# Performance work log

Hardware: AMD Instinct MI355X
Metric: run time of the kernel (lower is better)

## Reference

```python
import jax, jax.numpy as jnp
import numpy as np

C = 512
GROUPS = 32
EPS = 1e-6


def group_norm(x, w, b):
    # x: [B, C, H, W]
    B, Cc, H, W = x.shape
    xg = x.reshape(B, GROUPS, Cc // GROUPS, H, W)
    mean = xg.mean(axis=(2, 3, 4), keepdims=True)
    var = xg.var(axis=(2, 3, 4), keepdims=True)
    xn = (xg - mean) * jax.lax.rsqrt(var + EPS)
    xn = xn.reshape(B, Cc, H, W)
    return xn * w[None, :, None, None] + b[None, :, None, None]


def conv1x1(x, w, b):
    # 1x1 conv == per-pixel linear: w [Cout, Cin], x [B, Cin, H, W]
    return jnp.einsum('oc,bchw->bohw', w, x) + b[None, :, None, None]


def setup_inputs() -> dict:
    key = jax.random.key(0)
    ks = jax.random.split(key, 11)
    B, H, W = 4, 64, 64
    s = 1.0 / np.sqrt(C)
    return {
        'x': jax.random.normal(ks[0], (B, C, H, W), dtype=jnp.float32),
        'gn_w': jnp.ones((C,), dtype=jnp.float32),
        'gn_b': jnp.zeros((C,), dtype=jnp.float32),
        'wq': jax.random.normal(ks[1], (C, C), dtype=jnp.float32) * s,
        'bq': jnp.zeros((C,), dtype=jnp.float32),
        'wk': jax.random.normal(ks[2], (C, C), dtype=jnp.float32) * s,
        'bk': jnp.zeros((C,), dtype=jnp.float32),
        'wv': jax.random.normal(ks[3], (C, C), dtype=jnp.float32) * s,
        'bv': jnp.zeros((C,), dtype=jnp.float32),
        'wo': jax.random.normal(ks[4], (C, C), dtype=jnp.float32) * s,
        'bo': jnp.zeros((C,), dtype=jnp.float32),
    }


def reference(x, gn_w, gn_b, wq, bq, wk, bk, wv, bv, wo, bo):
    B, Cc, H, W = x.shape
    scale = Cc ** (-0.5)
    xn = group_norm(x, gn_w, gn_b)
    q = conv1x1(xn, wq, bq).reshape(B, Cc, H * W)
    k = conv1x1(xn, wk, bk).reshape(B, Cc, H * W)
    v = conv1x1(xn, wv, bv).reshape(B, Cc, H * W)
    attn = jax.nn.softmax(jnp.einsum('bci,bcj->bij', q, k) * scale, axis=2)
    out = jnp.einsum('bij,bcj->bci', attn, v).reshape(B, Cc, H, W)
    out = conv1x1(out, wo, bo)
    return x + out
```

## Files before the change

### kernel.cpp

```cpp
#include <hip/hip_runtime.h>

#define NB 4
#define CC 512
#define NSP 4096
#define NGRP 32

using bf16x8 = __attribute__((ext_vector_type(8))) __bf16;
using f32x4  = __attribute__((ext_vector_type(4))) float;

__device__ __forceinline__ unsigned short f2bf(float f) {
  union { float f; unsigned int u; } v; v.f = f;
  unsigned int r = v.u + 0x7fffu + ((v.u >> 16) & 1u);
  return (unsigned short)(r >> 16);
}
__device__ __forceinline__ float bf2f(unsigned short h) {
  union { unsigned int u; float f; } v; v.u = ((unsigned int)h) << 16;
  return v.f;
}

__global__ __launch_bounds__(256) void cvt_w_kernel(const float* __restrict__ wq,
    const float* __restrict__ wk, const float* __restrict__ wv,
    const float* __restrict__ wo, const float* __restrict__ bq,
    const float* __restrict__ bk, unsigned short* __restrict__ wqk,
    unsigned short* __restrict__ wv_bf, unsigned short* __restrict__ wo_bf,
    float* __restrict__ bias_qk, float scale) {
  int i = blockIdx.x * 256 + threadIdx.x;
  wqk[i]          = f2bf(wq[i] * scale);
  wqk[i + 262144] = f2bf(wk[i]);
  wv_bf[i] = f2bf(wv[i]);
  wo_bf[i] = f2bf(wo[i]);
  if (i < 512)        bias_qk[i] = bq[i] * scale;
  else if (i < 1024)  bias_qk[i] = bk[i - 512];
}

__global__ __launch_bounds__(256) void gn_stats_kernel(const float* __restrict__ x,
                                                       float* __restrict__ stats) {
  const int b = blockIdx.x >> 5, g = blockIdx.x & 31;
  const float4* p = reinterpret_cast<const float4*>(x + ((size_t)b * CC + g * 16) * NSP);
  float s = 0.f, ss = 0.f;
  for (int i = threadIdx.x; i < 16384; i += 256) {
    float4 v = p[i];
    s  += v.x + v.y + v.z + v.w;
    ss += v.x * v.x + v.y * v.y + v.z * v.z + v.w * v.w;
  }
  __shared__ float rs[4], rss[4];
  #pragma unroll
  for (int o = 32; o >= 1; o >>= 1) { s += __shfl_down(s, o); ss += __shfl_down(ss, o); }
  if ((threadIdx.x & 63) == 0) { rs[threadIdx.x >> 6] = s; rss[threadIdx.x >> 6] = ss; }
  __syncthreads();
  if (threadIdx.x == 0) {
    s = rs[0] + rs[1] + rs[2] + rs[3];
    ss = rss[0] + rss[1] + rss[2] + rss[3];
    float mean = s * (1.f / 65536.f);
    float var = ss * (1.f / 65536.f) - mean * mean;
    stats[blockIdx.x * 2 + 0] = mean;
    stats[blockIdx.x * 2 + 1] = rsqrtf(var + 1e-6f);
  }
}

__global__ __launch_bounds__(256) void gn_apply_kernel(const float* __restrict__ x,
    const float* __restrict__ stats, const float* __restrict__ gw,
    const float* __restrict__ gb, unsigned short* __restrict__ xnT) {
  const int b = blockIdx.z, c0 = blockIdx.y * 32, n0 = blockIdx.x * 32;
  __shared__ unsigned short tile[32][33];
  const int tx = threadIdx.x & 31, ty = threadIdx.x >> 5;
  #pragma unroll
  for (int r = 0; r < 4; ++r) {
    const int cl = ty + r * 8;
    const int c = c0 + cl;
    const int g = c >> 4;
    const float mean = stats[(b * 32 + g) * 2];
    const float rstd = stats[(b * 32 + g) * 2 + 1];
    const float sc = rstd * gw[c];
    const float sh = gb[c] - mean * sc;
    const float v = x[((size_t)b * CC + c) * NSP + n0 + tx];
    tile[cl][tx] = f2bf(v * sc + sh);
  }
  __syncthreads();
  #pragma unroll
  for (int r = 0; r < 4; ++r) {
    const int nl = ty + r * 8;
    xnT[((size_t)b * NSP + n0 + nl) * CC + c0 + tx] = tile[tx][nl];
  }
}

__global__ __launch_bounds__(256) void sum_reduce_kernel(const float* __restrict__ part,
                                                         float* __restrict__ invl) {
  const int row = blockIdx.x * 4 + (threadIdx.x >> 6);
  const int lane = threadIdx.x & 63;
  float v = part[((size_t)row << 6) + lane];
  #pragma unroll
  for (int msk = 1; msk <= 32; msk <<= 1) v += __shfl_xor(v, msk);
  if (lane == 0) invl[row] = 1.f / v;
}

template<int BIAS, int OMODE, bool RESID>
__global__ __launch_bounds__(256) void gemm2(
    const unsigned short* __restrict__ A, const unsigned short* __restrict__ B,
    const float* __restrict__ bias, const float* __restrict__ resid,
    void* __restrict__ Cout, void* __restrict__ Cout2,
    int M, int N, int K, float scale,
    long long sAb, long long sBb, long long sCb, long long sRb) {
  __shared__ __align__(16) unsigned short sA[2][128 * 64];
  __shared__ __align__(16) unsigned short sB[2][128 * 64];
  const int tid = threadIdx.x;
  const int lane = tid & 63;
  const int wid  = tid >> 6;

  const unsigned nwg = gridDim.x * gridDim.y * gridDim.z;
  unsigned lin = blockIdx.x + gridDim.x * (blockIdx.y + gridDim.y * blockIdx.z);
  lin = (lin & 7) * (nwg >> 3) + (lin >> 3);
  const int bn = lin % gridDim.x;
  const unsigned t2 = lin / gridDim.x;
  const int bm = t2 % gridDim.y;
  const int b  = t2 / gridDim.y;

  const unsigned short* Ab = A + (size_t)b * sAb + (size_t)bm * 128 * K;
  const unsigned short* Bb = B + (size_t)b * sBb + (size_t)bn * 128 * K;
  const int wm = wid >> 1, wn = wid & 1;
  const int l15 = lane & 15, h = lane >> 4;

  f32x4 acc[4][4] = {};

  auto stage = [&](int buf, int k0) {
    #pragma unroll
    for (int it = 0; it < 4; ++it) {
      const int o  = (it * 256 + tid) * 16;
      const int r  = o >> 7;
      const int c2 = (o & 127) ^ ((r & 7) << 4);
      __builtin_amdgcn_global_load_lds(
          (const __attribute__((address_space(1))) void*)((const char*)(Ab + (size_t)r * K + k0) + c2),
          (__attribute__((address_space(3))) void*)((char*)sA[buf] + o), 16, 0, 0);
      __builtin_amdgcn_global_load_lds(
          (const __attribute__((address_space(1))) void*)((const char*)(Bb + (size_t)r * K + k0) + c2),
          (__attribute__((address_space(3))) void*)((char*)sB[buf] + o), 16, 0, 0);
    }
  };

  int abase[4], bbase[4];
  #pragma unroll
  for (int i = 0; i < 4; ++i) {
    const int ar = wm * 64 + i * 16 + l15;
    abase[i] = ar * 128 + (((ar & 7) << 4) ^ (h << 4));
    const int br = wn * 64 + i * 16 + l15;
    bbase[i] = br * 128 + (((br & 7) << 4) ^ (h << 4));
  }

  stage(0, 0);
  const int NT = K >> 6;
  #pragma unroll 1
  for (int t = 0; t < NT; ++t) {
    const int cur = t & 1;
    if (t + 1 < NT) {
      stage(cur ^ 1, (t + 1) << 6);
      asm volatile("s_waitcnt vmcnt(8)" ::: "memory");
    } else {
      asm volatile("s_waitcnt vmcnt(0)" ::: "memory");
    }
    __builtin_amdgcn_sched_barrier(0);
    __builtin_amdgcn_s_barrier();
    __builtin_amdgcn_sched_barrier(0);

    const char* cA = (const char*)sA[cur];
    const char* cB = (const char*)sB[cur];
    #pragma unroll
    for (int kk = 0; kk < 2; ++kk) {
      bf16x8 af[4], bfr[4];
      #pragma unroll
      for (int m = 0; m < 4; ++m)
        af[m] = *reinterpret_cast<const bf16x8*>(cA + (abase[m] ^ (kk << 6)));
      #pragma unroll
      for (int n = 0; n < 4; ++n)
        bfr[n] = *reinterpret_cast<const bf16x8*>(cB + (bbase[n] ^ (kk << 6)));
      #pragma unroll
      for (int m = 0; m < 4; ++m)
        #pragma unroll
        for (int n = 0; n < 4; ++n)
          acc[m][n] = __builtin_amdgcn_mfma_f32_16x16x32_bf16(af[m], bfr[n], acc[m][n], 0, 0, 0);
    }
    __builtin_amdgcn_sched_barrier(0);
    __builtin_amdgcn_s_barrier();
    __builtin_amdgcn_sched_barrier(0);
  }

  const size_t cb = (size_t)b * sCb;
  #pragma unroll
  for (int m = 0; m < 4; ++m) {
    #pragma unroll
    for (int r = 0; r < 4; ++r) {
      const int row = bm * 128 + wm * 64 + m * 16 + h * 4 + r;
      #pragma unroll
      for (int n = 0; n < 4; ++n) {
        const int col = bn * 128 + wn * 64 + n * 16 + l15;
        float vv = acc[m][n][r];
        if constexpr (BIAS == 1) vv += bias[row];
        if constexpr (BIAS == 2) vv += bias[col];
        vv *= scale;
        if constexpr (RESID) vv += resid[(size_t)b * sRb + (size_t)row * N + col];
        if constexpr (OMODE == 0) {
          ((float*)Cout)[cb + (size_t)row * N + col] = vv;
        } else if constexpr (OMODE == 1) {
          ((unsigned short*)Cout)[cb + (size_t)row * N + col] = f2bf(vv);
        } else {
          unsigned short* dst = (col < 512) ? (unsigned short*)Cout : (unsigned short*)Cout2;
          dst[cb + (size_t)row * 512 + (col & 511)] = f2bf(vv);
        }
      }
    }
  }
}

template<int BN, int WMs, int OMODE>
__global__ __launch_bounds__(512) void gemm8p(
    const unsigned short* __restrict__ A, const unsigned short* __restrict__ B,
    void* __restrict__ Cout, const float* __restrict__ invl_in,
    float* __restrict__ part_out, int N, int K, int lda, int ldb,
    long long sAb, long long sBb, long long sCb) {
  constexpr int WNs = 8 / WMs;
  constexpr int WR = 256 / WMs;
  constexpr int M_REP = WR / 16;
  constexpr int BH = BN / 128;
  __shared__ __align__(16) unsigned short sA[2][256 * 64];
  __shared__ __align__(16) unsigned short sB[2][BN * 64];
  const int tid = threadIdx.x;
  const int lane = tid & 63;
  const int wid  = tid >> 6;

  const unsigned nwg = gridDim.x * gridDim.y * gridDim.z;
  unsigned lin = blockIdx.x + gridDim.x * (blockIdx.y + gridDim.y * blockIdx.z);
  lin = (lin & 7) * (nwg >> 3) + (lin >> 3);
  const int bn = lin % gridDim.x;
  const unsigned t2 = lin / gridDim.x;
  const int bm = t2 % gridDim.y;
  const int b  = t2 / gridDim.y;

  const unsigned short* Ab = A + (size_t)b * sAb + (size_t)bm * 256 * lda;
  const unsigned short* Bb = B + (size_t)b * sBb + (size_t)bn * BN * ldb;
  const int wm = wid / WNs, wn = wid % WNs;
  const int l15 = lane & 15, h = lane >> 4;

  auto stage_half = [&](const unsigned short* gbase, int ld, int k0, unsigned short* lbase) {
    #pragma unroll
    for (int it = 0; it < 2; ++it) {
      const int o = (it * 512 + tid) * 16;
      const int r = o >> 7;
      const int c2 = (o & 127) ^ ((r & 7) << 4);
      __builtin_amdgcn_global_load_lds(
          (const __attribute__((address_space(1))) void*)((const char*)(gbase + (size_t)r * ld + k0) + c2),
          (__attribute__((address_space(3))) void*)((char*)lbase + o), 16, 0, 0);
    }
  };

  int abase[M_REP], bbase[4];
  #pragma unroll
  for (int i = 0; i < M_REP; ++i) {
    const int ar = wm * WR + i * 16 + l15;
    abase[i] = ar * 128 + (((ar & 7) << 4) ^ (h << 4));
  }
  #pragma unroll
  for (int i = 0; i < 4; ++i) {
    const int br = wn * 64 + i * 16 + l15;
    bbase[i] = br * 128 + (((br & 7) << 4) ^ (h << 4));
  }

  f32x4 acc[M_REP][4] = {};
  const int NT = K >> 6;

  stage_half(Ab, lda, 0, &sA[0][0]);
  stage_half(Ab + (size_t)128 * lda, lda, 0, &sA[0][128 * 64]);
  #pragma unroll
  for (int hs = 0; hs < BH; ++hs)
    stage_half(Bb + (size_t)hs * 128 * ldb, ldb, 0, &sB[0][hs * 128 * 64]);
  #pragma unroll
  for (int hs = 0; hs < BH; ++hs)
    stage_half(Bb + (size_t)hs * 128 * ldb, ldb, 64, &sB[1][hs * 128 * 64]);
  if constexpr (BH == 2) asm volatile("s_waitcnt vmcnt(4)" ::: "memory");
  else                   asm volatile("s_waitcnt vmcnt(2)" ::: "memory");
  __builtin_amdgcn_s_barrier();

  #pragma unroll 1
  for (int u = 0; u < NT; u += 2) {
    const bool lastit = (u + 2 >= NT);
    #pragma unroll
    for (int half = 0; half < 2; ++half) {
      const char* cA = (const char*)sA[half];
      const char* cB = (const char*)sB[half];
      bf16x8 bfr[2][4];
      #pragma unroll
      for (int p = 0; p < M_REP / 2; ++p) {
        if (p == 0) {
          #pragma unroll
          for (int kk = 0; kk < 2; ++kk)
            #pragma unroll
            for (int n = 0; n < 4; ++n)
              bfr[kk][n] = *reinterpret_cast<const bf16x8*>(cB + (bbase[n] ^ (kk << 6)));
        }
        bf16x8 af[2][2];
        #pragma unroll
        for (int i = 0; i < 2; ++i)
          #pragma unroll
          for (int kk = 0; kk < 2; ++kk)
            af[kk][i] = *reinterpret_cast<const bf16x8*>(cA + (abase[2 * p + i] ^ (kk << 6)));

        const int ph = half * (M_REP / 2) + p;
        if constexpr (M_REP == 8) {
          if (ph == 0)      stage_half(Ab, lda, (u + 1) << 6, &sA[1][0]);
          else if (ph == 1) stage_half(Ab + (size_t)128 * lda, lda, (u + 1) << 6, &sA[1][128 * 64]);
          else if (ph == 2) { if (u + 2 < NT) stage_half(Bb, ldb, (u + 2) << 6, &sB[0][0]); }
          else if (ph == 3) { if (u + 2 < NT) stage_half(Bb + (size_t)128 * ldb, ldb, (u + 2) << 6, &sB[0][128 * 64]); }
          else if (ph == 4) { if (u + 2 < NT) stage_half(Ab, lda, (u + 2) << 6, &sA[0][0]); }
          else if (ph == 5) { if (u + 2 < NT) stage_half(Ab + (size_t)128 * lda, lda, (u + 2) << 6, &sA[0][128 * 64]); }
          else if (ph == 6) { if (u + 3 < NT) stage_half(Bb, ldb, (u + 3) << 6, &sB[1][0]); }
          else              { if (u + 3 < NT) stage_half(Bb + (size_t)128 * ldb, ldb, (u + 3) << 6, &sB[1][128 * 64]); }
        } else {
          if (ph == 0) {
            stage_half(Ab, lda, (u + 1) << 6, &sA[1][0]);
            stage_half(Ab + (size_t)128 * lda, lda, (u + 1) << 6, &sA[1][128 * 64]);
          } else if (ph == 1) {
            if (u + 2 < NT) stage_half(Bb, ldb, (u + 2) << 6, &sB[0][0]);
          } else if (ph == 2) {
            if (u + 2 < NT) {
              stage_half(Ab, lda, (u + 2) << 6, &sA[0][0]);
              stage_half(Ab + (size_t)128 * lda, lda, (u + 2) << 6, &sA[0][128 * 64]);
            }
          } else {
            if (u + 3 < NT) stage_half(Bb, ldb, (u + 3) << 6, &sB[1][0]);
          }
        }

        __builtin_amdgcn_s_barrier();
        asm volatile("s_waitcnt lgkmcnt(0)");
        __builtin_amdgcn_s_setprio(1);
        #pragma unroll
        for (int i = 0; i < 2; ++i)
          #pragma unroll
          for (int n = 0; n < 4; ++n)
            #pragma unroll
            for (int kk = 0; kk < 2; ++kk)
              acc[2 * p + i][n] = __builtin_amdgcn_mfma_f32_16x16x32_bf16(
                  af[kk][i], bfr[kk][n], acc[2 * p + i][n], 0, 0, 0);
        __builtin_amdgcn_s_setprio(0);
        if (p == M_REP / 2 - 1) {
          if (half == 0) {
            if (lastit) asm volatile("s_waitcnt vmcnt(0)" ::: "memory");
            else if constexpr (BH == 2) asm volatile("s_waitcnt vmcnt(4)" ::: "memory");
            else                        asm volatile("s_waitcnt vmcnt(2)" ::: "memory");
          } else if (!lastit) {
            if constexpr (BH == 2) asm volatile("s_waitcnt vmcnt(4)" ::: "memory");
            else                   asm volatile("s_waitcnt vmcnt(2)" ::: "memory");
          }
        }
        __builtin_amdgcn_s_barrier();
      }
    }
  }

  const size_t cb = (size_t)b * sCb;
  if constexpr (OMODE == 2) {
    unsigned short* outh = (unsigned short*)Cout;
    #pragma unroll
    for (int m = 0; m < M_REP; ++m) {
      #pragma unroll
      for (int r = 0; r < 4; ++r) {
        const int row = bm * 256 + wm * WR + m * 16 + h * 4 + r;
        float se = 0.f;
        #pragma unroll
        for (int n = 0; n < 4; ++n) {
          const int col = bn * BN + wn * 64 + n * 16 + l15;
          unsigned short pb = f2bf(__expf(fminf(acc[m][n][r], 80.f)));
          outh[cb + (size_t)row * N + col] = pb;
          se += bf2f(pb);
        }
        #pragma unroll
        for (int msk = 1; msk <= 8; msk <<= 1) se += __shfl_xor(se, msk);
        if (l15 == 0)
          part_out[(((size_t)b * NSP + row) << 6) + bn * (BN / 64) + wn] = se;
      }
    }
  } else {
    unsigned short* outh = (unsigned short*)Cout;
    #pragma unroll
    for (int m = 0; m < M_REP; ++m) {
      #pragma unroll
      for (int r = 0; r < 4; ++r) {
        const int row = bm * 256 + wm * WR + m * 16 + h * 4 + r;
        const float il = invl_in[(size_t)b * NSP + row];
        #pragma unroll
        for (int n = 0; n < 4; ++n) {
          const int col = bn * BN + wn * 64 + n * 16 + l15;
          outh[cb + (size_t)row * N + col] = f2bf(acc[m][n][r] * il);
        }
      }
    }
  }
}

extern "C" void kernel_launch(void* const* d_in, const int* in_sizes, int n_in,
                              void* d_out, int out_size, void* d_ws, size_t ws_size,
                              hipStream_t stream) {
  const float* x    = (const float*)d_in[0];
  const float* gn_w = (const float*)d_in[1];
  const float* gn_b = (const float*)d_in[2];
  const float* wq   = (const float*)d_in[3];
  const float* bq   = (const float*)d_in[4];
  const float* wk   = (const float*)d_in[5];
  const float* bk   = (const float*)d_in[6];
  const float* wv   = (const float*)d_in[7];
  const float* bv   = (const float*)d_in[8];
  const float* wo   = (const float*)d_in[9];
  const float* bo   = (const float*)d_in[10];
  float* out = (float*)d_out;

  char* ws = (char*)d_ws;
  const size_t NC = (size_t)NSP * CC;
  unsigned short* wqk_bf = (unsigned short*)ws;
  unsigned short* wv_bf  = wqk_bf + 524288;
  unsigned short* wo_bf  = wv_bf + 262144;
  float* bias_qk = (float*)(wo_bf + 262144);
  float* gstats  = bias_qk + 1024;
  unsigned short* xnT = (unsigned short*)(gstats + 512);
  unsigned short* qT  = xnT + NB * NC;
  unsigned short* kT  = qT + NB * NC;
  unsigned short* vC  = kT + NB * NC;
  unsigned short* aoutT = vC + NB * NC;
  unsigned short* S = aoutT + NB * NC;
  float* part = (float*)(S + (size_t)NB * NSP * NSP);
  float* invl = part + ((size_t)NB * NSP << 6);

  const float scale = 0.04419417382415922f;
  const long long SS = (long long)NSP * NSP;

  cvt_w_kernel<<<1024, 256, 0, stream>>>(wq, wk, wv, wo, bq, bk,
                                         wqk_bf, wv_bf, wo_bf, bias_qk, scale);
  gn_stats_kernel<<<NB * NGRP, 256, 0, stream>>>(x, gstats);
  gn_apply_kernel<<<dim3(NSP / 32, CC / 32, NB), 256, 0, stream>>>(x, gstats, gn_w, gn_b, xnT);

  gemm2<2, 3, false><<<dim3(1024 / 128, NSP / 128, NB), 256, 0, stream>>>(
      xnT, wqk_bf, bias_qk, nullptr, qT, kT, NSP, 1024, CC, 1.0f, NC, 0, NC, 0);
  gemm2<1, 1, false><<<dim3(NSP / 128, CC / 128, NB), 256, 0, stream>>>(
      wv_bf, xnT, bv, nullptr, vC, nullptr, CC, NSP, CC, 1.0f, 0, NC, NC, 0);

  gemm8p<256, 2, 2><<<dim3(NSP / 256, NSP / 256, NB), 512, 0, stream>>>(
      qT, kT, S, nullptr, part, NSP, CC, CC, CC, NC, NC, SS);
  sum_reduce_kernel<<<NB * NSP / 4, 256, 0, stream>>>(part, invl);
  gemm8p<128, 4, 1><<<dim3(CC / 128, NSP / 256, NB), 512, 0, stream>>>(
      S, vC, aoutT, invl, nullptr, CC, NSP, NSP, NSP, SS, NC, NC);

  gemm2<1, 0, true><<<dim3(NSP / 128, CC / 128, NB), 256, 0, stream>>>(
      wo_bf, aoutT, bo, x, out, nullptr, CC, NSP, CC, 1.0f, 0, NC, NC, NC);
}
```

Baseline: 280.5 us.

## Transpose attention GEMMs to emit vectorized ushort4 stores and halve partial sums

Swaps the operand roles of the QK^T and PV GEMMs so the score matrix is computed transposed (rows index keys, columns index queries). Each thread can then write four consecutive bf16 exponentials as one ushort4 store instead of scattered 2-byte stores. Row-sum partials now accumulate along the key dimension in registers with fewer shuffles, giving 32 partials per row instead of 64, and the reduction kernel is adjusted to match. The PV GEMM grid and operand strides are reworked to consume the transposed S layout. The risk is that the new index mapping does not line up exactly with the S layout and part-slot count the kernels assume.

```diff
diff --git a/kernel.cpp b/kernel.cpp
--- a/kernel.cpp
+++ b/kernel.cpp
@@ -86,12 +86,12 @@
 
 __global__ __launch_bounds__(256) void sum_reduce_kernel(const float* __restrict__ part,
                                                          float* __restrict__ invl) {
-  const int row = blockIdx.x * 4 + (threadIdx.x >> 6);
-  const int lane = threadIdx.x & 63;
-  float v = part[((size_t)row << 6) + lane];
-  #pragma unroll
-  for (int msk = 1; msk <= 32; msk <<= 1) v += __shfl_xor(v, msk);
-  if (lane == 0) invl[row] = 1.f / v;
+  const int row = blockIdx.x * 8 + (threadIdx.x >> 5);
+  const int sl = threadIdx.x & 31;
+  float v = part[((size_t)row << 5) + sl];
+  #pragma unroll
+  for (int msk = 1; msk <= 16; msk <<= 1) v += __shfl_xor(v, msk);
+  if (sl == 0) invl[row] = 1.f / v;
 }
 
 template<int BIAS, int OMODE, bool RESID>
@@ -358,38 +358,49 @@
   const size_t cb = (size_t)b * sCb;
   if constexpr (OMODE == 2) {
     unsigned short* outh = (unsigned short*)Cout;
+    float pn[4] = {0.f, 0.f, 0.f, 0.f};
     #pragma unroll
     for (int m = 0; m < M_REP; ++m) {
-      #pragma unroll
-      for (int r = 0; r < 4; ++r) {
-        const int row = bm * 256 + wm * WR + m * 16 + h * 4 + r;
-        float se = 0.f;
-        #pragma unroll
-        for (int n = 0; n < 4; ++n) {
-          const int col = bn * BN + wn * 64 + n * 16 + l15;
-          unsigned short pb = f2bf(__expf(fminf(acc[m][n][r], 80.f)));
-          outh[cb + (size_t)row * N + col] = pb;
-          se += bf2f(pb);
-        }
-        #pragma unroll
-        for (int msk = 1; msk <= 8; msk <<= 1) se += __shfl_xor(se, msk);
-        if (l15 == 0)
-          part_out[(((size_t)b * NSP + row) << 6) + bn * (BN / 64) + wn] = se;
+      const int j0 = bm * 256 + wm * WR + m * 16 + h * 4;
+      #pragma unroll
+      for (int n = 0; n < 4; ++n) {
+        const int i = bn * BN + wn * 64 + n * 16 + l15;
+        ushort4 pk;
+        pk.x = f2bf(__expf(fminf(acc[m][n][0], 80.f)));
+        pk.y = f2bf(__expf(fminf(acc[m][n][1], 80.f)));
+        pk.z = f2bf(__expf(fminf(acc[m][n][2], 80.f)));
+        pk.w = f2bf(__expf(fminf(acc[m][n][3], 80.f)));
+        *reinterpret_cast<ushort4*>(&outh[cb + (size_t)i * N + j0]) = pk;
+        pn[n] += bf2f(pk.x) + bf2f(pk.y) + bf2f(pk.z) + bf2f(pk.w);
+      }
+    }
+    #pragma unroll
+    for (int n = 0; n < 4; ++n) {
+      pn[n] += __shfl_xor(pn[n], 16);
+      pn[n] += __shfl_xor(pn[n], 32);
+    }
+    if (lane < 16) {
+      #pragma unroll
+      for (int n = 0; n < 4; ++n) {
+        const int i = bn * BN + wn * 64 + n * 16 + lane;
+        part_out[(((size_t)b * NSP + i) << 5) + bm * 2 + wm] = pn[n];
       }
     }
   } else {
     unsigned short* outh = (unsigned short*)Cout;
     #pragma unroll
-    for (int m = 0; m < M_REP; ++m) {
-      #pragma unroll
-      for (int r = 0; r < 4; ++r) {
-        const int row = bm * 256 + wm * WR + m * 16 + h * 4 + r;
-        const float il = invl_in[(size_t)b * NSP + row];
-        #pragma unroll
-        for (int n = 0; n < 4; ++n) {
-          const int col = bn * BN + wn * 64 + n * 16 + l15;
-          outh[cb + (size_t)row * N + col] = f2bf(acc[m][n][r] * il);
-        }
+    for (int n = 0; n < 4; ++n) {
+      const int i = bn * BN + wn * 64 + n * 16 + l15;
+      const float il = invl_in[(size_t)b * NSP + i];
+      #pragma unroll
+      for (int m = 0; m < M_REP; ++m) {
+        const int c0 = bm * 256 + wm * WR + m * 16 + h * 4;
+        ushort4 pk;
+        pk.x = f2bf(acc[m][n][0] * il);
+        pk.y = f2bf(acc[m][n][1] * il);
+        pk.z = f2bf(acc[m][n][2] * il);
+        pk.w = f2bf(acc[m][n][3] * il);
+        *reinterpret_cast<ushort4*>(&outh[cb + (size_t)i * N + c0]) = pk;
       }
     }
   }
@@ -425,7 +436,7 @@
   unsigned short* aoutT = vC + NB * NC;
   unsigned short* S = aoutT + NB * NC;
   float* part = (float*)(S + (size_t)NB * NSP * NSP);
-  float* invl = part + ((size_t)NB * NSP << 6);
+  float* invl = part + ((size_t)NB * NSP << 5);
 
   const float scale = 0.04419417382415922f;
   const long long SS = (long long)NSP * NSP;
@@ -441,10 +452,10 @@
       wv_bf, xnT, bv, nullptr, vC, nullptr, CC, NSP, CC, 1.0f, 0, NC, NC, 0);
 
   gemm8p<256, 2, 2><<<dim3(NSP / 256, NSP / 256, NB), 512, 0, stream>>>(
-      qT, kT, S, nullptr, part, NSP, CC, CC, CC, NC, NC, SS);
-  sum_reduce_kernel<<<NB * NSP / 4, 256, 0, stream>>>(part, invl);
-  gemm8p<128, 4, 1><<<dim3(CC / 128, NSP / 256, NB), 512, 0, stream>>>(
-      S, vC, aoutT, invl, nullptr, CC, NSP, NSP, NSP, SS, NC, NC);
+      kT, qT, S, nullptr, part, NSP, CC, CC, CC, NC, NC, SS);
+  sum_reduce_kernel<<<NB * NSP / 8, 256, 0, stream>>>(part, invl);
+  gemm8p<128, 4, 1><<<dim3(NSP / 128, CC / 256, NB), 512, 0, stream>>>(
+      vC, S, aoutT, invl, nullptr, CC, NSP, NSP, NSP, NC, SS, NC);
 
   gemm2<1, 0, true><<<dim3(NSP / 128, CC / 128, NB), 256, 0, stream>>>(
       wo_bf, aoutT, bo, x, out, nullptr, CC, NSP, CC, 1.0f, 0, NC, NC, NC);
```

After: 286.9 us. 2.3% more time.

## Switch attention GEMMs to 32x32x16 MFMA with k-chunk-major LDS layout

Applied to the files above, without the earlier changes.

Replaces the 16x16x32 bf16 MFMA tiling in the two large attention GEMMs with 32x32x16 MFMA. Each wave now holds fewer, larger accumulator blocks, which cuts the fragment loads from LDS per unit of math. The LDS staging layout changes from a row-major XOR-swizzled tile to a k-chunk-major layout ([kchunk][row] of 16-byte vectors) that suits the 32-lane fragment reads. The epilogues (exp plus row-sum partials, and the 1/l normalization) are rewritten for the 32x32 accumulator register layout. The risks are LDS bank conflicts from the unswizzled layout and different register pressure.

```diff
diff --git a/kernel.cpp b/kernel.cpp
--- a/kernel.cpp
+++ b/kernel.cpp
@@ -7,6 +7,7 @@
 
 using bf16x8 = __attribute__((ext_vector_type(8))) __bf16;
 using f32x4  = __attribute__((ext_vector_type(4))) float;
+using f32x16 = __attribute__((ext_vector_type(16))) float;
 
 __device__ __forceinline__ unsigned short f2bf(float f) {
   union { float f; unsigned int u; } v; v.f = f;
@@ -211,17 +212,17 @@
 }
 
 template<int BN, int WMs, int OMODE>
-__global__ __launch_bounds__(512) void gemm8p(
+__global__ __launch_bounds__(512) void gemm32(
     const unsigned short* __restrict__ A, const unsigned short* __restrict__ B,
     void* __restrict__ Cout, const float* __restrict__ invl_in,
     float* __restrict__ part_out, int N, int K, int lda, int ldb,
     long long sAb, long long sBb, long long sCb) {
   constexpr int WNs = 8 / WMs;
   constexpr int WR = 256 / WMs;
-  constexpr int M_REP = WR / 16;
+  constexpr int MB = WR / 32;
   constexpr int BH = BN / 128;
-  __shared__ __align__(16) unsigned short sA[2][256 * 64];
-  __shared__ __align__(16) unsigned short sB[2][BN * 64];
+  __shared__ __align__(16) unsigned short sA[2][8 * 256 * 8];
+  __shared__ __align__(16) unsigned short sB[2][8 * BN * 8];
   const int tid = threadIdx.x;
   const int lane = tid & 63;
   const int wid  = tid >> 6;
@@ -237,43 +238,39 @@
   const unsigned short* Ab = A + (size_t)b * sAb + (size_t)bm * 256 * lda;
   const unsigned short* Bb = B + (size_t)b * sBb + (size_t)bn * BN * ldb;
   const int wm = wid / WNs, wn = wid % WNs;
-  const int l15 = lane & 15, h = lane >> 4;
-
-  auto stage_half = [&](const unsigned short* gbase, int ld, int k0, unsigned short* lbase) {
+  const int l31 = lane & 31, hsel = lane >> 5;
+
+  auto stage_seg = [&](const unsigned short* gbase, int ld, int k0, int hs,
+                       unsigned short* lbase, int R) {
     #pragma unroll
     for (int it = 0; it < 2; ++it) {
-      const int o = (it * 512 + tid) * 16;
-      const int r = o >> 7;
-      const int c2 = (o & 127) ^ ((r & 7) << 4);
+      const int c = it * 512 + tid;
+      const int kh = c >> 7, r = c & 127;
+      const int row = hs * 128 + r;
       __builtin_amdgcn_global_load_lds(
-          (const __attribute__((address_space(1))) void*)((const char*)(gbase + (size_t)r * ld + k0) + c2),
-          (__attribute__((address_space(3))) void*)((char*)lbase + o), 16, 0, 0);
+          (const __attribute__((address_space(1))) void*)(
+              (const char*)(gbase + (size_t)row * ld + k0) + kh * 16),
+          (__attribute__((address_space(3))) void*)(
+              (char*)lbase + (size_t)(kh * R + row) * 16),
+          16, 0, 0);
     }
   };
 
-  int abase[M_REP], bbase[4];
-  #pragma unroll
-  for (int i = 0; i < M_REP; ++i) {
-    const int ar = wm * WR + i * 16 + l15;
-    abase[i] = ar * 128 + (((ar & 7) << 4) ^ (h << 4));
-  }
-  #pragma unroll
-  for (int i = 0; i < 4; ++i) {
-    const int br = wn * 64 + i * 16 + l15;
-    bbase[i] = br * 128 + (((br & 7) << 4) ^ (h << 4));
-  }
-
-  f32x4 acc[M_REP][4] = {};
+  int arow[MB], brow[2];
+  #pragma unroll
+  for (int i = 0; i < MB; ++i) arow[i] = wm * WR + i * 32 + l31;
+  #pragma unroll
+  for (int i = 0; i < 2; ++i) brow[i] = wn * 64 + i * 32 + l31;
+
+  f32x16 acc[MB][2] = {};
   const int NT = K >> 6;
 
-  stage_half(Ab, lda, 0, &sA[0][0]);
-  stage_half(Ab + (size_t)128 * lda, lda, 0, &sA[0][128 * 64]);
-  #pragma unroll
-  for (int hs = 0; hs < BH; ++hs)
-    stage_half(Bb + (size_t)hs * 128 * ldb, ldb, 0, &sB[0][hs * 128 * 64]);
-  #pragma unroll
-  for (int hs = 0; hs < BH; ++hs)
-    stage_half(Bb + (size_t)hs * 128 * ldb, ldb, 64, &sB[1][hs * 128 * 64]);
+  stage_seg(Ab, lda, 0, 0, sA[0], 256);
+  stage_seg(Ab, lda, 0, 1, sA[0], 256);
+  #pragma unroll
+  for (int hs = 0; hs < BH; ++hs) stage_seg(Bb, ldb, 0, hs, sB[0], BN);
+  #pragma unroll
+  for (int hs = 0; hs < BH; ++hs) stage_seg(Bb, ldb, 64, hs, sB[1], BN);
   if constexpr (BH == 2) asm volatile("s_waitcnt vmcnt(4)" ::: "memory");
   else                   asm volatile("s_waitcnt vmcnt(2)" ::: "memory");
   __builtin_amdgcn_s_barrier();
@@ -287,44 +284,44 @@
       const char* cB = (const char*)sB[half];
       bf16x8 bfr[2][4];
       #pragma unroll
-      for (int p = 0; p < M_REP / 2; ++p) {
+      for (int p = 0; p < MB; ++p) {
         if (p == 0) {
           #pragma unroll
-          for (int kk = 0; kk < 2; ++kk)
+          for (int nb = 0; nb < 2; ++nb)
             #pragma unroll
-            for (int n = 0; n < 4; ++n)
-              bfr[kk][n] = *reinterpret_cast<const bf16x8*>(cB + (bbase[n] ^ (kk << 6)));
+            for (int kk = 0; kk < 4; ++kk)
+              bfr[nb][kk] = *reinterpret_cast<const bf16x8*>(
+                  cB + (size_t)((kk * 2 + hsel) * BN + brow[nb]) * 16);
         }
-        bf16x8 af[2][2];
+        bf16x8 af[4];
         #pragma unroll
-        for (int i = 0; i < 2; ++i)
-          #pragma unroll
-          for (int kk = 0; kk < 2; ++kk)
-            af[kk][i] = *reinterpret_cast<const bf16x8*>(cA + (abase[2 * p + i] ^ (kk << 6)));
-
-        const int ph = half * (M_REP / 2) + p;
-        if constexpr (M_REP == 8) {
-          if (ph == 0)      stage_half(Ab, lda, (u + 1) << 6, &sA[1][0]);
-          else if (ph == 1) stage_half(Ab + (size_t)128 * lda, lda, (u + 1) << 6, &sA[1][128 * 64]);
-          else if (ph == 2) { if (u + 2 < NT) stage_half(Bb, ldb, (u + 2) << 6, &sB[0][0]); }
-          else if (ph == 3) { if (u + 2 < NT) stage_half(Bb + (size_t)128 * ldb, ldb, (u + 2) << 6, &sB[0][128 * 64]); }
-          else if (ph == 4) { if (u + 2 < NT) stage_half(Ab, lda, (u + 2) << 6, &sA[0][0]); }
-          else if (ph == 5) { if (u + 2 < NT) stage_half(Ab + (size_t)128 * lda, lda, (u + 2) << 6, &sA[0][128 * 64]); }
-          else if (ph == 6) { if (u + 3 < NT) stage_half(Bb, ldb, (u + 3) << 6, &sB[1][0]); }
-          else              { if (u + 3 < NT) stage_half(Bb + (size_t)128 * ldb, ldb, (u + 3) << 6, &sB[1][128 * 64]); }
+        for (int kk = 0; kk < 4; ++kk)
+          af[kk] = *reinterpret_cast<const bf16x8*>(
+              cA + (size_t)((kk * 2 + hsel) * 256 + arow[p]) * 16);
+
+        const int ph = half * MB + p;
+        if constexpr (MB == 4) {
+          if (ph == 0)      stage_seg(Ab, lda, (u + 1) << 6, 0, sA[1], 256);
+          else if (ph == 1) stage_seg(Ab, lda, (u + 1) << 6, 1, sA[1], 256);
+          else if (ph == 2) { if (u + 2 < NT) stage_seg(Bb, ldb, (u + 2) << 6, 0, sB[0], BN); }
+          else if (ph == 3) { if (u + 2 < NT) stage_seg(Bb, ldb, (u + 2) << 6, 1, sB[0], BN); }
+          else if (ph == 4) { if (u + 2 < NT) stage_seg(Ab, lda, (u + 2) << 6, 0, sA[0], 256); }
+          else if (ph == 5) { if (u + 2 < NT) stage_seg(Ab, lda, (u + 2) << 6, 1, sA[0], 256); }
+          else if (ph == 6) { if (u + 3 < NT) stage_seg(Bb, ldb, (u + 3) << 6, 0, sB[1], BN); }
+          else              { if (u + 3 < NT) stage_seg(Bb, ldb, (u + 3) << 6, 1, sB[1], BN); }
         } else {
           if (ph == 0) {
-            stage_half(Ab, lda, (u + 1) << 6, &sA[1][0]);
-            stage_half(Ab + (size_t)128 * lda, lda, (u + 1) << 6, &sA[1][128 * 64]);
+            stage_seg(Ab, lda, (u + 1) << 6, 0, sA[1], 256);
+            stage_seg(Ab, lda, (u + 1) << 6, 1, sA[1], 256);
           } else if (ph == 1) {
-            if (u + 2 < NT) stage_half(Bb, ldb, (u + 2) << 6, &sB[0][0]);
+            if (u + 2 < NT) stage_seg(Bb, ldb, (u + 2) << 6, 0, sB[0], BN);
           } else if (ph == 2) {
             if (u + 2 < NT) {
-              stage_half(Ab, lda, (u + 2) << 6, &sA[0][0]);
-              stage_half(Ab + (size_t)128 * lda, lda, (u + 2) << 6, &sA[0][128 * 64]);
+              stage_seg(Ab, lda, (u + 2) << 6, 0, sA[0], 256);
+              stage_seg(Ab, lda, (u + 2) << 6, 1, sA[0], 256);
             }
           } else {
-            if (u + 3 < NT) stage_half(Bb, ldb, (u + 3) << 6, &sB[1][0]);
+            if (u + 3 < NT) stage_seg(Bb, ldb, (u + 3) << 6, 0, sB[1], BN);
           }
         }
 
@@ -332,15 +329,13 @@
         asm volatile("s_waitcnt lgkmcnt(0)");
         __builtin_amdgcn_s_setprio(1);
         #pragma unroll
-        for (int i = 0; i < 2; ++i)
+        for (int nb = 0; nb < 2; ++nb)
           #pragma unroll
-          for (int n = 0; n < 4; ++n)
-            #pragma unroll
-            for (int kk = 0; kk < 2; ++kk)
-              acc[2 * p + i][n] = __builtin_amdgcn_mfma_f32_16x16x32_bf16(
-                  af[kk][i], bfr[kk][n], acc[2 * p + i][n], 0, 0, 0);
+          for (int kk = 0; kk < 4; ++kk)
+            acc[p][nb] = __builtin_amdgcn_mfma_f32_32x32x16_bf16(
+                af[kk], bfr[nb][kk], acc[p][nb], 0, 0, 0);
         __builtin_amdgcn_s_setprio(0);
-        if (p == M_REP / 2 - 1) {
+        if (p == MB - 1) {
           if (half == 0) {
             if (lastit) asm volatile("s_waitcnt vmcnt(0)" ::: "memory");
             else if constexpr (BH == 2) asm volatile("s_waitcnt vmcnt(4)" ::: "memory");
@@ -356,40 +351,35 @@
   }
 
   const size_t cb = (size_t)b * sCb;
+  unsigned short* outh = (unsigned short*)Cout;
+  const int col0 = bn * BN + wn * 64 + l31;
   if constexpr (OMODE == 2) {
-    unsigned short* outh = (unsigned short*)Cout;
-    #pragma unroll
-    for (int m = 0; m < M_REP; ++m) {
-      #pragma unroll
-      for (int r = 0; r < 4; ++r) {
-        const int row = bm * 256 + wm * WR + m * 16 + h * 4 + r;
-        float se = 0.f;
+    #pragma unroll
+    for (int mb = 0; mb < MB; ++mb) {
+      #pragma unroll
+      for (int reg = 0; reg < 16; ++reg) {
+        const int row = bm * 256 + wm * WR + mb * 32 + (reg & 3) + 8 * (reg >> 2) + 4 * hsel;
+        float p0 = __expf(fminf(acc[mb][0][reg], 80.f));
+        float p1 = __expf(fminf(acc[mb][1][reg], 80.f));
+        unsigned short b0 = f2bf(p0), b1 = f2bf(p1);
+        outh[cb + (size_t)row * N + col0]      = b0;
+        outh[cb + (size_t)row * N + col0 + 32] = b1;
+        float s = bf2f(b0) + bf2f(b1);
         #pragma unroll
-        for (int n = 0; n < 4; ++n) {
-          const int col = bn * BN + wn * 64 + n * 16 + l15;
-          unsigned short pb = f2bf(__expf(fminf(acc[m][n][r], 80.f)));
-          outh[cb + (size_t)row * N + col] = pb;
-          se += bf2f(pb);
-        }
-        #pragma unroll
-        for (int msk = 1; msk <= 8; msk <<= 1) se += __shfl_xor(se, msk);
-        if (l15 == 0)
-          part_out[(((size_t)b * NSP + row) << 6) + bn * (BN / 64) + wn] = se;
+        for (int msk = 1; msk <= 16; msk <<= 1) s += __shfl_xor(s, msk);
+        if (l31 == 0)
+          part_out[(((size_t)b * NSP + row) << 6) + bn * WNs + wn] = s;
       }
     }
   } else {
-    unsigned short* outh = (unsigned short*)Cout;
-    #pragma unroll
-    for (int m = 0; m < M_REP; ++m) {
-      #pragma unroll
-      for (int r = 0; r < 4; ++r) {
-        const int row = bm * 256 + wm * WR + m * 16 + h * 4 + r;
+    #pragma unroll
+    for (int mb = 0; mb < MB; ++mb) {
+      #pragma unroll
+      for (int reg = 0; reg < 16; ++reg) {
+        const int row = bm * 256 + wm * WR + mb * 32 + (reg & 3) + 8 * (reg >> 2) + 4 * hsel;
         const float il = invl_in[(size_t)b * NSP + row];
-        #pragma unroll
-        for (int n = 0; n < 4; ++n) {
-          const int col = bn * BN + wn * 64 + n * 16 + l15;
-          outh[cb + (size_t)row * N + col] = f2bf(acc[m][n][r] * il);
-        }
+        outh[cb + (size_t)row * N + col0]      = f2bf(acc[mb][0][reg] * il);
+        outh[cb + (size_t)row * N + col0 + 32] = f2bf(acc[mb][1][reg] * il);
       }
     }
   }
@@ -440,10 +430,10 @@
   gemm2<1, 1, false><<<dim3(NSP / 128, CC / 128, NB), 256, 0, stream>>>(
       wv_bf, xnT, bv, nullptr, vC, nullptr, CC, NSP, CC, 1.0f, 0, NC, NC, 0);
 
-  gemm8p<256, 2, 2><<<dim3(NSP / 256, NSP / 256, NB), 512, 0, stream>>>(
+  gemm32<256, 2, 2><<<dim3(NSP / 256, NSP / 256, NB), 512, 0, stream>>>(
       qT, kT, S, nullptr, part, NSP, CC, CC, CC, NC, NC, SS);
   sum_reduce_kernel<<<NB * NSP / 4, 256, 0, stream>>>(part, invl);
-  gemm8p<128, 4, 1><<<dim3(CC / 128, NSP / 256, NB), 512, 0, stream>>>(
+  gemm32<128, 4, 1><<<dim3(CC / 128, NSP / 256, NB), 512, 0, stream>>>(
       S, vC, aoutT, invl, nullptr, CC, NSP, NSP, NSP, SS, NC, NC);
 
   gemm2<1, 0, true><<<dim3(NSP / 128, CC / 128, NB), 256, 0, stream>>>(
```

After: 367.1 us. 1.31x slower.
